# Performance work log

Measured on AMD Instinct MI355X. Metric: run time of the kernel, lower is better.

## Reference

```python
import jax, jax.numpy as jnp
import numpy as np

N = 50000
E = 800000
IN_C = 128
HID = 32
OUT_C = 16
NEG_SLOPE = 0.2


def setup_inputs() -> dict:
    key = jax.random.key(0)
    ks = jax.random.split(key, 16)
    x = jax.random.normal(ks[0], (N, IN_C), dtype=jnp.float32)
    edge_index = jax.random.randint(ks[1], (2, E), 0, N, dtype=jnp.int64)

    def glorot(k, shape):
        fan = shape[0] + shape[-1]
        return jax.random.uniform(k, shape, jnp.float32, -1.0, 1.0) * jnp.sqrt(6.0 / fan)

    # layer1: in=128 -> heads=4, ch=32, concat -> out 128
    W1 = glorot(ks[2], (IN_C, 4 * HID))
    a_src1 = glorot(ks[3], (4, HID))
    a_dst1 = glorot(ks[4], (4, HID))
    b1 = jnp.zeros((4 * HID,), jnp.float32)
    # layer2: in=128 -> heads=2, ch=32, concat -> out 64
    W2 = glorot(ks[5], (4 * HID, 2 * HID))
    a_src2 = glorot(ks[6], (2, HID))
    a_dst2 = glorot(ks[7], (2, HID))
    b2 = jnp.zeros((2 * HID,), jnp.float32)
    # layer3: in=64 -> heads=1, ch=16, mean -> out 16
    W3 = glorot(ks[8], (2 * HID, OUT_C))
    a_src3 = glorot(ks[9], (1, OUT_C))
    a_dst3 = glorot(ks[10], (1, OUT_C))
    b3 = jnp.zeros((OUT_C,), jnp.float32)
    return {"x": x, "edge_index": edge_index,
            "W1": W1, "a_src1": a_src1, "a_dst1": a_dst1, "b1": b1,
            "W2": W2, "a_src2": a_src2, "a_dst2": a_dst2, "b2": b2,
            "W3": W3, "a_src3": a_src3, "a_dst3": a_dst3, "b3": b3}


def gat_conv(x, src, dst, W, a_src, a_dst, bias, heads, ch, concat):
    n = x.shape[0]
    h = (x @ W).reshape(n, heads, ch)                      # [N,H,C]
    alpha_s = jnp.einsum('nhc,hc->nh', h, a_src)           # [N,H]
    alpha_d = jnp.einsum('nhc,hc->nh', h, a_dst)           # [N,H]
    logits = jax.nn.leaky_relu(alpha_s[src] + alpha_d[dst], NEG_SLOPE)  # [E,H]
    # segment softmax over edges sharing the same destination node
    m = jax.ops.segment_max(logits, dst, num_segments=n)
    m = jnp.where(jnp.isfinite(m), m, 0.0)
    e = jnp.exp(logits - m[dst])
    denom = jax.ops.segment_sum(e, dst, num_segments=n)
    alpha = e / (denom[dst] + 1e-16)                       # [E,H]
    msg = h[src] * alpha[:, :, None]                       # [E,H,C]
    out = jax.ops.segment_sum(msg, dst, num_segments=n)    # [N,H,C]
    out = out.reshape(n, heads * ch) if concat else out.mean(axis=1)
    return out + bias


def reference(x, edge_index, W1, a_src1, a_dst1, b1, W2, a_src2, a_dst2, b2, W3, a_src3, a_dst3, b3):
    n = x.shape[0]
    loops = jnp.arange(n, dtype=edge_index.dtype)
    src = jnp.concatenate([edge_index[0], loops])  # add self loops (PyG default)
    dst = jnp.concatenate([edge_index[1], loops])
    h = jax.nn.relu(gat_conv(x, src, dst, W1, a_src1, a_dst1, b1, 4, HID, True))
    h = jax.nn.relu(gat_conv(h, src, dst, W2, a_src2, a_dst2, b2, 2, HID, True))
    out = gat_conv(h, src, dst, W3, a_src3, a_dst3, b3, 1, OUT_C, False)
    return out
```

## Files before the change

### kernel.cpp

```cpp
#include <hip/hip_runtime.h>
#include <hip/hip_bf16.h>
#include <stdint.h>

#define NODES 50000
#define NEDGE 800000
#define TEDGE (NEDGE + NODES)

typedef unsigned short u16;
typedef unsigned int u32;
typedef unsigned long long u64;
typedef short s16x8 __attribute__((ext_vector_type(8)));
typedef float f32x4 __attribute__((ext_vector_type(4)));

__device__ __forceinline__ float bf2f(u16 v) {
  return __uint_as_float(((u32)v) << 16);
}
__device__ __forceinline__ u16 f2bf(float f) {
  u32 u = __float_as_uint(f);
  u32 r = (u + 0x7FFFu + ((u >> 16) & 1u)) >> 16;
  return (u16)r;
}
__device__ __forceinline__ float lrelu(float x) {
  return (x > 0.f) ? x : 0.2f * x;
}
__device__ __forceinline__ int clampn(int v) {
  return ((u32)v < NODES) ? v : 0;
}
__device__ __forceinline__ float load1(const void* p, size_t i, bool fb) {
  return fb ? bf2f(((const u16*)p)[i]) : ((const float*)p)[i];
}
__device__ __forceinline__ float bflo(u32 w) { return __uint_as_float(w << 16); }
__device__ __forceinline__ float bfhi(u32 w) { return __uint_as_float(w & 0xFFFF0000u); }
__device__ __forceinline__ u32 encf(float f) {
  u32 u = __float_as_uint(f);
  return (u & 0x80000000u) ? ~u : (u | 0x80000000u);
}
__device__ __forceinline__ float decf(u32 k) {
  u32 u = (k & 0x80000000u) ? (k & 0x7FFFFFFFu) : ~k;
  return __uint_as_float(u);
}
__device__ __forceinline__ void fma8(float* ac, uint4 v, float a) {
  ac[0] += a * bflo(v.x); ac[1] += a * bfhi(v.x);
  ac[2] += a * bflo(v.y); ac[3] += a * bfhi(v.y);
  ac[4] += a * bflo(v.z); ac[5] += a * bfhi(v.z);
  ac[6] += a * bflo(v.w); ac[7] += a * bfhi(v.w);
}

__global__ __launch_bounds__(256) void k_probe(const int* __restrict__ ei,
                                               const u16* __restrict__ xs16,
                                               int* __restrict__ flags,
                                               int* __restrict__ deg) {
  int t = threadIdx.x;
  int g = blockIdx.x * 256 + t;
  if (g < NODES) deg[g] = 0;
  if (blockIdx.x == 0 && t >= 2 && t < 32) flags[t] = 0;
  if (blockIdx.x == 0 && t < 64) {
    int odd = 0, even = 0, big = 0;
#pragma unroll
    for (int k = 0; k < 4; ++k) {
      int idx = t + 64 * k;
      odd |= (ei[2 * idx + 1] != 0);
      even |= (ei[2 * idx] != 0);
      u32 ex = (xs16[2 * (t * 4 + k)] >> 7) & 0xFF;
      big += (ex >= 0x90);
    }
    u64 bo = __ballot(odd);
    u64 be = __ballot(even);
#pragma unroll
    for (int off = 32; off >= 1; off >>= 1) big += __shfl_xor(big, off);
    if (t == 0) {
      flags[0] = (bo == 0ull && be != 0ull) ? 1 : 0;
      flags[1] = (big >= 8) ? 0 : 1;
    }
  }
}

__global__ __launch_bounds__(256) void k_tw(const void* __restrict__ W1,
                                            const void* __restrict__ W2,
                                            const void* __restrict__ W3,
                                            const int* __restrict__ flags,
                                            u16* __restrict__ wt1,
                                            u16* __restrict__ wt2,
                                            u16* __restrict__ wt3) {
  int id = blockIdx.x * 256 + threadIdx.x;
  bool fb = flags[1] != 0;
  if (id < 16384) {
    int n = id >> 7, k = id & 127;
    wt1[n * 128 + k] = f2bf(load1(W1, (size_t)k * 128 + n, fb));
  } else if (id < 24576) {
    int r = id - 16384;
    int n = r >> 7, k = r & 127;
    wt2[n * 128 + k] = f2bf(load1(W2, (size_t)k * 64 + n, fb));
  } else if (id < 25600) {
    int r = id - 24576;
    int n = r >> 6, k = r & 63;
    wt3[n * 64 + k] = f2bf(load1(W3, (size_t)k * 16 + n, fb));
  }
}


__global__ __launch_bounds__(256) void k_hist(const int* __restrict__ ei,
                                              const int* __restrict__ flags,
                                              int* deg, u16* __restrict__ rankarr) {
  int e = blockIdx.x * 256 + threadIdx.x;
  if (e >= TEDGE) return;
  int d;
  if (e < NEDGE) {
    d = flags[0] ? ei[2 * (NEDGE + e)] : ei[NEDGE + e];
  } else {
    d = e - NEDGE;
  }
  int r = atomicAdd(&deg[clampn(d)], 1);
  rankarr[e] = (u16)min(r, 65535);
}

__global__ __launch_bounds__(1024) void k_scan(const int* __restrict__ deg,
                                               int* __restrict__ rowptr, int n) {
  int t = threadIdx.x, lane = t & 63, w = t >> 6;
  __shared__ int swave[16], soff[17];
  int carry = 0;
  for (int base = 0; base < n; base += 4096) {
    int i0 = base + t * 4;
    int v[4];
#pragma unroll
    for (int j = 0; j < 4; j++) { int i = i0 + j; v[j] = (i < n) ? deg[i] : 0; }
    int local = v[0] + v[1] + v[2] + v[3];
    int x = local;
#pragma unroll
    for (int off = 1; off < 64; off <<= 1) {
      int y = __shfl_up(x, off);
      if (lane >= off) x += y;
    }
    if (lane == 63) swave[w] = x;
    __syncthreads();
    if (w == 0) {
      int wv = (lane < 16) ? swave[lane] : 0;
#pragma unroll
      for (int off = 1; off < 16; off <<= 1) {
        int y = __shfl_up(wv, off);
        if (lane >= off) wv += y;
      }
      if (lane < 16) soff[lane + 1] = wv;
      if (lane == 0) soff[0] = 0;
    }
    __syncthreads();
    int run = carry + soff[w] + (x - local);
#pragma unroll
    for (int j = 0; j < 4; j++) {
      int i = i0 + j;
      if (i < n) rowptr[i] = run;
      run += v[j];
    }
    carry += soff[16];
    __syncthreads();
  }
  if (t == 0) rowptr[n] = carry;
}

__global__ __launch_bounds__(256) void k_scatter(const int* __restrict__ ei,
                                                 const int* __restrict__ flags,
                                                 const int* __restrict__ rowptr,
                                                 const u16* __restrict__ rankarr,
                                                 u16* __restrict__ srcs) {
  int e = blockIdx.x * 256 + threadIdx.x;
  if (e >= TEDGE) return;
  int d, s;
  if (e < NEDGE) {
    if (flags[0]) { s = ei[2 * e]; d = ei[2 * (NEDGE + e)]; }
    else { s = ei[e]; d = ei[NEDGE + e]; }
  } else {
    s = e - NEDGE; d = s;
  }
  int pos = rowptr[clampn(d)] + (int)rankarr[e];
  srcs[pos] = (u16)clampn(s);
}


template <int K, int N, int H, bool XEXT>
__global__ __launch_bounds__(256) void k_gmfma(const void* __restrict__ xin,
                                               const u16* __restrict__ wtg,
                                               const void* __restrict__ a_src,
                                               const void* __restrict__ a_dst,
                                               u16* __restrict__ hout,
                                               float* __restrict__ asg,
                                               float* __restrict__ adg,
                                               u32* __restrict__ gm,
                                               const int* __restrict__ flags,
                                               int M) {
  constexpr int KP = K + 8;
  constexpr int NT = N / 16;
  constexpr int NTH = NT / H;
  constexpr int KG = K / 8;
  __shared__ u16 wlds[N * KP];
  __shared__ u16 xlds[64 * KP];
  __shared__ u32 lmax[2 * H];
  int t = threadIdx.x;
  int row0 = blockIdx.x * 64;
  bool fb = flags[1] != 0;
  if (t < 2 * H) lmax[t] = 0;

  for (int i = t; i < N * KG; i += 256) {
    int n = i / KG, kg = i % KG;
    *(uint4*)&wlds[n * KP + kg * 8] = *(const uint4*)(wtg + (size_t)n * K + kg * 8);
  }
  bool xbf = XEXT ? fb : true;
  for (int i = t; i < 64 * KG; i += 256) {
    int r = i / KG, kg = i % KG;
    int grow = row0 + r;
    if (grow >= M) grow = M - 1;
    if (xbf) {
      *(uint4*)&xlds[r * KP + kg * 8] =
          *(const uint4*)((const u16*)xin + (size_t)grow * K + kg * 8);
    } else {
      const float* gp = (const float*)xin + (size_t)grow * K + kg * 8;
      float4 f0 = *(const float4*)gp, f1 = *(const float4*)(gp + 4);
      *(ushort4*)&xlds[r * KP + kg * 8] =
          make_ushort4(f2bf(f0.x), f2bf(f0.y), f2bf(f0.z), f2bf(f0.w));
      *(ushort4*)&xlds[r * KP + kg * 8 + 4] =
          make_ushort4(f2bf(f1.x), f2bf(f1.y), f2bf(f1.z), f2bf(f1.w));
    }
  }
  __syncthreads();

  int lane = t & 63, w = t >> 6;
  int lrow = lane & 15, quad = lane >> 4;
  f32x4 acc[NT];
#pragma unroll
  for (int nt = 0; nt < NT; ++nt) acc[nt] = (f32x4){0.f, 0.f, 0.f, 0.f};

  const u16* xbase = xlds + (w * 16 + lrow) * KP + quad * 8;
  const u16* wbase = wlds + lrow * KP + quad * 8;
#pragma unroll
  for (int ks = 0; ks < K / 32; ++ks) {
    s16x8 a = *(const s16x8*)(xbase + ks * 32);
#pragma unroll
    for (int nt = 0; nt < NT; ++nt) {
      s16x8 b = *(const s16x8*)(wbase + (size_t)nt * 16 * KP + ks * 32);
      acc[nt] = __builtin_amdgcn_mfma_f32_16x16x32_bf16(a, b, acc[nt], 0, 0, 0);
    }
  }

  float avs[NT], avd[NT];
#pragma unroll
  for (int nt = 0; nt < NT; ++nt) {
    avs[nt] = load1(a_src, nt * 16 + lrow, fb);
    avd[nt] = load1(a_dst, nt * 16 + lrow, fb);
  }
  int baserow = row0 + w * 16 + quad * 4;
#pragma unroll
  for (int r = 0; r < 4; ++r) {
    int grow = baserow + r;
    float ps[H], pd[H];
#pragma unroll
    for (int h = 0; h < H; ++h) {
      ps[h] = 0.f; pd[h] = 0.f;
#pragma unroll
      for (int i = 0; i < NTH; ++i) {
        int nt = h * NTH + i;
        ps[h] += acc[nt][r] * avs[nt];
        pd[h] += acc[nt][r] * avd[nt];
      }
    }
#pragma unroll
    for (int m = 1; m < 16; m <<= 1) {
#pragma unroll
      for (int h = 0; h < H; ++h) {
        ps[h] += __shfl_xor(ps[h], m);
        pd[h] += __shfl_xor(pd[h], m);
      }
    }
    if (grow < M) {
#pragma unroll
      for (int nt = 0; nt < NT; ++nt)
        hout[(size_t)grow * N + nt * 16 + lrow] = f2bf(acc[nt][r]);
#pragma unroll
      for (int h = 0; h < H; ++h) {
        if (lrow == h) {
          asg[grow * H + h] = ps[h];
          adg[grow * H + h] = pd[h];
          atomicMax(&lmax[h], encf(ps[h]));
          atomicMax(&lmax[H + h], encf(pd[h]));
        }
      }
    }
  }
  __syncthreads();
  if (t < 2 * H) atomicMax(&gm[t], lmax[t]);
}


template <int H, int C, bool RELU, bool FINAL>
__global__ __launch_bounds__(256) void k_agg(const u16* __restrict__ hbuf,
                                             const float* __restrict__ asg,
                                             const float* __restrict__ adg,
                                             const int* __restrict__ rowptr,
                                             const u16* __restrict__ srcs,
                                             const void* __restrict__ bias,
                                             const int* __restrict__ flags,
                                             const u32* __restrict__ gm,
                                             void* __restrict__ outp, int n) {
  constexpr int HC = H * C;
  constexpr int L = HC / 8;
  constexpr int EPN = 32 / L;
  constexpr int UN = (4 * EPN <= 32) ? 4 : 2;
  __shared__ u16 lds_s[4][64];
  __shared__ float lds_e[4][64][H];
  int lane = threadIdx.x & 63;
  int w = threadIdx.x >> 6;
  int nh = lane >> 5;
  int hl = lane & 31;
  int node = blockIdx.x * 8 + w * 2 + nh;
  if (node >= n) node = n - 1;
  bool fb = flags[1] != 0;
  int start = rowptr[node], end = rowptr[node + 1];
  if (end < start || end - start > TEDGE) { start = 0; end = 0; }

  float adh[H], M[H];
#pragma unroll
  for (int h = 0; h < H; ++h) adh[h] = adg[node * H + h];
#pragma unroll
  for (int h = 0; h < H; ++h) M[h] = lrelu(decf(gm[h]) + decf(gm[H + h]));

  int sub = hl / L;
  int cl = hl & (L - 1);
  int ch0 = cl * 8;
  int myhead = ch0 / C;
  int base = nh * 32;

  float den[H];
#pragma unroll
  for (int h = 0; h < H; ++h) den[h] = 0.f;
  float acc[UN][8];
#pragma unroll
  for (int u = 0; u < UN; ++u)
#pragma unroll
    for (int i = 0; i < 8; ++i) acc[u][i] = 0.f;

  for (int chunk = start; chunk < end; chunk += 32) {
    int e = chunk + hl;
    int s = 0;
    float ee[H];
#pragma unroll
    for (int h = 0; h < H; ++h) ee[h] = 0.f;
    if (e < end) {
      s = srcs[e];
      float av[H];
      if (H == 4) { float4 t4 = *(const float4*)(asg + s * 4);
        av[0] = t4.x; av[1] = t4.y; av[H > 2 ? 2 : 0] = t4.z; av[H > 3 ? 3 : 0] = t4.w; }
      else if (H == 2) { float2 t2 = *(const float2*)(asg + s * 2); av[0] = t2.x; av[1] = t2.y; }
      else av[0] = asg[s];
#pragma unroll
      for (int h = 0; h < H; ++h) {
        float x = __expf(lrelu(av[h] + adh[h]) - M[h]);
        ee[h] = x;
        den[h] += x;
      }
    }
    __builtin_amdgcn_wave_barrier();
    lds_s[w][lane] = (u16)s;
#pragma unroll
    for (int h = 0; h < H; ++h) lds_e[w][lane][h] = ee[h];
    __builtin_amdgcn_wave_barrier();

    int cn = min(32, end - chunk);
    for (int j = 0; j < cn; j += UN * EPN) {
      int sx[UN];
      float ax[UN];
#pragma unroll
      for (int u = 0; u < UN; ++u) {
        int ei_ = base + j + u * EPN + sub;
        sx[u] = lds_s[w][ei_];
        ax[u] = lds_e[w][ei_][myhead];
      }
#pragma unroll
      for (int u = 0; u < UN; ++u) {
        uint4 v = *(const uint4*)(hbuf + (size_t)sx[u] * HC + ch0);
        fma8(acc[u], v, ax[u]);
      }
    }
  }

#pragma unroll
  for (int m = 16; m >= 1; m >>= 1) {
#pragma unroll
    for (int h = 0; h < H; ++h) den[h] += __shfl_xor(den[h], m);
  }
  float tt[8];
#pragma unroll
  for (int i = 0; i < 8; ++i) {
    tt[i] = acc[0][i];
#pragma unroll
    for (int u = 1; u < UN; ++u) tt[i] += acc[u][i];
  }
#pragma unroll
  for (int m = L; m < 32; m <<= 1) {
#pragma unroll
    for (int i = 0; i < 8; ++i) tt[i] += __shfl_xor(tt[i], m);
  }

  if (sub == 0) {
    float inv = 1.f / (den[myhead] + 1e-16f);
    float o[8];
#pragma unroll
    for (int i = 0; i < 8; ++i) {
      o[i] = tt[i] * inv + load1(bias, ch0 + i, fb);
      if (RELU) o[i] = fmaxf(o[i], 0.f);
    }
    bool obf = FINAL ? fb : true;
    if (obf) {
      uint4 pk;
      pk.x = (u32)f2bf(o[0]) | ((u32)f2bf(o[1]) << 16);
      pk.y = (u32)f2bf(o[2]) | ((u32)f2bf(o[3]) << 16);
      pk.z = (u32)f2bf(o[4]) | ((u32)f2bf(o[5]) << 16);
      pk.w = (u32)f2bf(o[6]) | ((u32)f2bf(o[7]) << 16);
      *(uint4*)((u16*)outp + (size_t)node * HC + ch0) = pk;
    } else {
      float* op = (float*)outp + (size_t)node * HC + ch0;
      *(float4*)op = make_float4(o[0], o[1], o[2], o[3]);
      *(float4*)(op + 4) = make_float4(o[4], o[5], o[6], o[7]);
    }
  }
}


extern "C" void kernel_launch(void* const* d_in, const int* in_sizes, int n_in,
                              void* d_out, int out_size, void* d_ws, size_t ws_size,
                              hipStream_t stream) {
  const void* x   = d_in[0];
  const int* ei   = (const int*)d_in[1];
  const void* W1  = d_in[2];
  const void* as1 = d_in[3];
  const void* ad1 = d_in[4];
  const void* b1  = d_in[5];
  const void* W2  = d_in[6];
  const void* as2 = d_in[7];
  const void* ad2 = d_in[8];
  const void* b2  = d_in[9];
  const void* W3  = d_in[10];
  const void* as3 = d_in[11];
  const void* ad3 = d_in[12];
  const void* b3  = d_in[13];

  char* w = (char*)d_ws;
  auto alloc = [&](size_t bytes) {
    char* p = w;
    w += (bytes + 255) & ~(size_t)255;
    return p;
  };
  int* flags    = (int*)alloc(256);
  int* deg      = (int*)alloc((size_t)NODES * 4);
  int* rowptr   = (int*)alloc((size_t)(NODES + 1) * 4);
  u16* rankarr  = (u16*)alloc((size_t)TEDGE * 2);
  u16* srcs     = (u16*)alloc((size_t)TEDGE * 2);
  float* asg    = (float*)alloc((size_t)NODES * 4 * 4);
  float* adg    = (float*)alloc((size_t)NODES * 4 * 4);
  u16* wt1      = (u16*)alloc((size_t)128 * 128 * 2);
  u16* wt2      = (u16*)alloc((size_t)64 * 128 * 2);
  u16* wt3      = (u16*)alloc((size_t)16 * 64 * 2);
  u16* hbuf     = (u16*)alloc((size_t)NODES * 128 * 2);
  u16* obuf     = (u16*)alloc((size_t)NODES * 128 * 2);

  u32* gm1 = (u32*)(flags + 8);
  u32* gm2 = (u32*)(flags + 16);
  u32* gm3 = (u32*)(flags + 24);

  k_probe<<<(NODES + 255) / 256, 256, 0, stream>>>(ei, (const u16*)x, flags, deg);
  k_tw<<<100, 256, 0, stream>>>(W1, W2, W3, flags, wt1, wt2, wt3);
  k_hist<<<(TEDGE + 255) / 256, 256, 0, stream>>>(ei, flags, deg, rankarr);
  k_scan<<<1, 1024, 0, stream>>>(deg, rowptr, NODES);
  k_scatter<<<(TEDGE + 255) / 256, 256, 0, stream>>>(ei, flags, rowptr, rankarr, srcs);

  int gblocks = (NODES + 63) / 64;
  int ablocks = (NODES + 7) / 8;
  k_gmfma<128, 128, 4, true><<<gblocks, 256, 0, stream>>>(x, wt1, as1, ad1, hbuf, asg, adg, gm1, flags, NODES);
  k_agg<4, 32, true, false><<<ablocks, 256, 0, stream>>>(hbuf, asg, adg, rowptr, srcs, b1, flags, gm1, obuf, NODES);
  k_gmfma<128, 64, 2, false><<<gblocks, 256, 0, stream>>>(obuf, wt2, as2, ad2, hbuf, asg, adg, gm2, flags, NODES);
  k_agg<2, 32, true, false><<<ablocks, 256, 0, stream>>>(hbuf, asg, adg, rowptr, srcs, b2, flags, gm2, obuf, NODES);
  k_gmfma<64, 16, 1, false><<<gblocks, 256, 0, stream>>>(obuf, wt3, as3, ad3, hbuf, asg, adg, gm3, flags, NODES);
  k_agg<1, 16, false, true><<<ablocks, 256, 0, stream>>>(hbuf, asg, adg, rowptr, srcs, b3, flags, gm3, d_out, NODES);
}
```

Measured before the change: 310.4 us.

## Switch intermediates to fp16 MFMA and cache compact edge indices for scatter

Moves the weight, projected-feature and intermediate activation buffers from bf16 to fp16, so the GEMMs use the f16 MFMA variant and aggregation decodes fp16 halves, which gives more mantissa precision. The histogram kernel now writes clamped 16-bit source and destination arrays, so the scatter pass reads 4 bytes per edge instead of re-reading the 64-bit edge_index. This adds two extra writes per edge in k_hist and a float conversion cost per element in the aggregation loop. fp16 also risks overflow if activations grow large.

```diff
diff --git a/kernel.cpp b/kernel.cpp
--- a/kernel.cpp
+++ b/kernel.cpp
@@ -9,7 +9,8 @@
 typedef unsigned short u16;
 typedef unsigned int u32;
 typedef unsigned long long u64;
-typedef short s16x8 __attribute__((ext_vector_type(8)));
+typedef _Float16 f16;
+typedef _Float16 f16x8 __attribute__((ext_vector_type(8)));
 typedef float f32x4 __attribute__((ext_vector_type(4)));
 
 __device__ __forceinline__ float bf2f(u16 v) {
@@ -20,6 +21,18 @@
   u32 r = (u + 0x7FFFu + ((u >> 16) & 1u)) >> 16;
   return (u16)r;
 }
+__device__ __forceinline__ u16 f2h(float f) {
+  return __builtin_bit_cast(u16, (f16)f);
+}
+__device__ __forceinline__ float h2f(u16 b) {
+  return (float)__builtin_bit_cast(f16, b);
+}
+__device__ __forceinline__ float lo16f(u32 w) {
+  return (float)__builtin_bit_cast(f16, (u16)(w & 0xFFFFu));
+}
+__device__ __forceinline__ float hi16f(u32 w) {
+  return (float)__builtin_bit_cast(f16, (u16)(w >> 16));
+}
 __device__ __forceinline__ float lrelu(float x) {
   return (x > 0.f) ? x : 0.2f * x;
 }
@@ -29,8 +42,6 @@
 __device__ __forceinline__ float load1(const void* p, size_t i, bool fb) {
   return fb ? bf2f(((const u16*)p)[i]) : ((const float*)p)[i];
 }
-__device__ __forceinline__ float bflo(u32 w) { return __uint_as_float(w << 16); }
-__device__ __forceinline__ float bfhi(u32 w) { return __uint_as_float(w & 0xFFFF0000u); }
 __device__ __forceinline__ u32 encf(float f) {
   u32 u = __float_as_uint(f);
   return (u & 0x80000000u) ? ~u : (u | 0x80000000u);
@@ -39,11 +50,11 @@
   u32 u = (k & 0x80000000u) ? (k & 0x7FFFFFFFu) : ~k;
   return __uint_as_float(u);
 }
-__device__ __forceinline__ void fma8(float* ac, uint4 v, float a) {
-  ac[0] += a * bflo(v.x); ac[1] += a * bfhi(v.x);
-  ac[2] += a * bflo(v.y); ac[3] += a * bfhi(v.y);
-  ac[4] += a * bflo(v.z); ac[5] += a * bfhi(v.z);
-  ac[6] += a * bflo(v.w); ac[7] += a * bfhi(v.w);
+__device__ __forceinline__ void fma8h(float* ac, uint4 v, float a) {
+  ac[0] += a * lo16f(v.x); ac[1] += a * hi16f(v.x);
+  ac[2] += a * lo16f(v.y); ac[3] += a * hi16f(v.y);
+  ac[4] += a * lo16f(v.z); ac[5] += a * hi16f(v.z);
+  ac[6] += a * lo16f(v.w); ac[7] += a * hi16f(v.w);
 }
 
 __global__ __launch_bounds__(256) void k_probe(const int* __restrict__ ei,
@@ -86,31 +97,37 @@
   bool fb = flags[1] != 0;
   if (id < 16384) {
     int n = id >> 7, k = id & 127;
-    wt1[n * 128 + k] = f2bf(load1(W1, (size_t)k * 128 + n, fb));
+    wt1[n * 128 + k] = f2h(load1(W1, (size_t)k * 128 + n, fb));
   } else if (id < 24576) {
     int r = id - 16384;
     int n = r >> 7, k = r & 127;
-    wt2[n * 128 + k] = f2bf(load1(W2, (size_t)k * 64 + n, fb));
+    wt2[n * 128 + k] = f2h(load1(W2, (size_t)k * 64 + n, fb));
   } else if (id < 25600) {
     int r = id - 24576;
     int n = r >> 6, k = r & 63;
-    wt3[n * 64 + k] = f2bf(load1(W3, (size_t)k * 16 + n, fb));
+    wt3[n * 64 + k] = f2h(load1(W3, (size_t)k * 16 + n, fb));
   }
 }
 
 
 __global__ __launch_bounds__(256) void k_hist(const int* __restrict__ ei,
                                               const int* __restrict__ flags,
-                                              int* deg, u16* __restrict__ rankarr) {
+                                              int* deg, u16* __restrict__ rankarr,
+                                              u16* __restrict__ src16,
+                                              u16* __restrict__ dst16) {
   int e = blockIdx.x * 256 + threadIdx.x;
   if (e >= TEDGE) return;
-  int d;
+  int d, s;
   if (e < NEDGE) {
-    d = flags[0] ? ei[2 * (NEDGE + e)] : ei[NEDGE + e];
+    if (flags[0]) { s = ei[2 * e]; d = ei[2 * (NEDGE + e)]; }
+    else { s = ei[e]; d = ei[NEDGE + e]; }
   } else {
-    d = e - NEDGE;
-  }
-  int r = atomicAdd(&deg[clampn(d)], 1);
+    s = e - NEDGE; d = s;
+  }
+  s = clampn(s); d = clampn(d);
+  src16[e] = (u16)s;
+  dst16[e] = (u16)d;
+  int r = atomicAdd(&deg[d], 1);
   rankarr[e] = (u16)min(r, 65535);
 }
 
@@ -157,22 +174,16 @@
   if (t == 0) rowptr[n] = carry;
 }
 
-__global__ __launch_bounds__(256) void k_scatter(const int* __restrict__ ei,
-                                                 const int* __restrict__ flags,
+__global__ __launch_bounds__(256) void k_scatter(const u16* __restrict__ src16,
+                                                 const u16* __restrict__ dst16,
                                                  const int* __restrict__ rowptr,
                                                  const u16* __restrict__ rankarr,
                                                  u16* __restrict__ srcs) {
   int e = blockIdx.x * 256 + threadIdx.x;
   if (e >= TEDGE) return;
-  int d, s;
-  if (e < NEDGE) {
-    if (flags[0]) { s = ei[2 * e]; d = ei[2 * (NEDGE + e)]; }
-    else { s = ei[e]; d = ei[NEDGE + e]; }
-  } else {
-    s = e - NEDGE; d = s;
-  }
-  int pos = rowptr[clampn(d)] + (int)rankarr[e];
-  srcs[pos] = (u16)clampn(s);
+  int d = dst16[e];
+  int pos = rowptr[d] + (int)rankarr[e];
+  srcs[pos] = src16[e];
 }
 
 
@@ -203,21 +214,29 @@
     int n = i / KG, kg = i % KG;
     *(uint4*)&wlds[n * KP + kg * 8] = *(const uint4*)(wtg + (size_t)n * K + kg * 8);
   }
-  bool xbf = XEXT ? fb : true;
   for (int i = t; i < 64 * KG; i += 256) {
     int r = i / KG, kg = i % KG;
     int grow = row0 + r;
     if (grow >= M) grow = M - 1;
-    if (xbf) {
+    if (XEXT) {
+      if (fb) {
+        const u16* gp = (const u16*)xin + (size_t)grow * K + kg * 8;
+        ushort4 v0 = *(const ushort4*)gp, v1 = *(const ushort4*)(gp + 4);
+        *(ushort4*)&xlds[r * KP + kg * 8] = make_ushort4(
+            f2h(bf2f(v0.x)), f2h(bf2f(v0.y)), f2h(bf2f(v0.z)), f2h(bf2f(v0.w)));
+        *(ushort4*)&xlds[r * KP + kg * 8 + 4] = make_ushort4(
+            f2h(bf2f(v1.x)), f2h(bf2f(v1.y)), f2h(bf2f(v1.z)), f2h(bf2f(v1.w)));
+      } else {
+        const float* gp = (const float*)xin + (size_t)grow * K + kg * 8;
+        float4 f0 = *(const float4*)gp, f1 = *(const float4*)(gp + 4);
+        *(ushort4*)&xlds[r * KP + kg * 8] =
+            make_ushort4(f2h(f0.x), f2h(f0.y), f2h(f0.z), f2h(f0.w));
+        *(ushort4*)&xlds[r * KP + kg * 8 + 4] =
+            make_ushort4(f2h(f1.x), f2h(f1.y), f2h(f1.z), f2h(f1.w));
+      }
+    } else {
       *(uint4*)&xlds[r * KP + kg * 8] =
           *(const uint4*)((const u16*)xin + (size_t)grow * K + kg * 8);
-    } else {
-      const float* gp = (const float*)xin + (size_t)grow * K + kg * 8;
-      float4 f0 = *(const float4*)gp, f1 = *(const float4*)(gp + 4);
-      *(ushort4*)&xlds[r * KP + kg * 8] =
-          make_ushort4(f2bf(f0.x), f2bf(f0.y), f2bf(f0.z), f2bf(f0.w));
-      *(ushort4*)&xlds[r * KP + kg * 8 + 4] =
-          make_ushort4(f2bf(f1.x), f2bf(f1.y), f2bf(f1.z), f2bf(f1.w));
     }
   }
   __syncthreads();
@@ -232,11 +251,11 @@
   const u16* wbase = wlds + lrow * KP + quad * 8;
 #pragma unroll
   for (int ks = 0; ks < K / 32; ++ks) {
-    s16x8 a = *(const s16x8*)(xbase + ks * 32);
+    f16x8 a = *(const f16x8*)(xbase + ks * 32);
 #pragma unroll
     for (int nt = 0; nt < NT; ++nt) {
-      s16x8 b = *(const s16x8*)(wbase + (size_t)nt * 16 * KP + ks * 32);
-      acc[nt] = __builtin_amdgcn_mfma_f32_16x16x32_bf16(a, b, acc[nt], 0, 0, 0);
+      f16x8 b = *(const f16x8*)(wbase + (size_t)nt * 16 * KP + ks * 32);
+      acc[nt] = __builtin_amdgcn_mfma_f32_16x16x32_f16(a, b, acc[nt], 0, 0, 0);
     }
   }
 
@@ -272,7 +291,7 @@
     if (grow < M) {
 #pragma unroll
       for (int nt = 0; nt < NT; ++nt)
-        hout[(size_t)grow * N + nt * 16 + lrow] = f2bf(acc[nt][r]);
+        hout[(size_t)grow * N + nt * 16 + lrow] = f2h(acc[nt][r]);
 #pragma unroll
       for (int h = 0; h < H; ++h) {
         if (lrow == h) {
@@ -375,7 +394,7 @@
 #pragma unroll
       for (int u = 0; u < UN; ++u) {
         uint4 v = *(const uint4*)(hbuf + (size_t)sx[u] * HC + ch0);
-        fma8(acc[u], v, ax[u]);
+        fma8h(acc[u], v, ax[u]);
       }
     }
   }
@@ -406,18 +425,26 @@
       o[i] = tt[i] * inv + load1(bias, ch0 + i, fb);
       if (RELU) o[i] = fmaxf(o[i], 0.f);
     }
-    bool obf = FINAL ? fb : true;
-    if (obf) {
+    if (FINAL) {
+      if (fb) {
+        uint4 pk;
+        pk.x = (u32)f2bf(o[0]) | ((u32)f2bf(o[1]) << 16);
+        pk.y = (u32)f2bf(o[2]) | ((u32)f2bf(o[3]) << 16);
+        pk.z = (u32)f2bf(o[4]) | ((u32)f2bf(o[5]) << 16);
+        pk.w = (u32)f2bf(o[6]) | ((u32)f2bf(o[7]) << 16);
+        *(uint4*)((u16*)outp + (size_t)node * HC + ch0) = pk;
+      } else {
+        float* op = (float*)outp + (size_t)node * HC + ch0;
+        *(float4*)op = make_float4(o[0], o[1], o[2], o[3]);
+        *(float4*)(op + 4) = make_float4(o[4], o[5], o[6], o[7]);
+      }
+    } else {
       uint4 pk;
-      pk.x = (u32)f2bf(o[0]) | ((u32)f2bf(o[1]) << 16);
-      pk.y = (u32)f2bf(o[2]) | ((u32)f2bf(o[3]) << 16);
-      pk.z = (u32)f2bf(o[4]) | ((u32)f2bf(o[5]) << 16);
-      pk.w = (u32)f2bf(o[6]) | ((u32)f2bf(o[7]) << 16);
+      pk.x = (u32)f2h(o[0]) | ((u32)f2h(o[1]) << 16);
+      pk.y = (u32)f2h(o[2]) | ((u32)f2h(o[3]) << 16);
+      pk.z = (u32)f2h(o[4]) | ((u32)f2h(o[5]) << 16);
+      pk.w = (u32)f2h(o[6]) | ((u32)f2h(o[7]) << 16);
       *(uint4*)((u16*)outp + (size_t)node * HC + ch0) = pk;
-    } else {
-      float* op = (float*)outp + (size_t)node * HC + ch0;
-      *(float4*)op = make_float4(o[0], o[1], o[2], o[3]);
-      *(float4*)(op + 4) = make_float4(o[4], o[5], o[6], o[7]);
     }
   }
 }
@@ -451,6 +478,8 @@
   int* deg      = (int*)alloc((size_t)NODES * 4);
   int* rowptr   = (int*)alloc((size_t)(NODES + 1) * 4);
   u16* rankarr  = (u16*)alloc((size_t)TEDGE * 2);
+  u16* src16    = (u16*)alloc((size_t)TEDGE * 2);
+  u16* dst16    = (u16*)alloc((size_t)TEDGE * 2);
   u16* srcs     = (u16*)alloc((size_t)TEDGE * 2);
   float* asg    = (float*)alloc((size_t)NODES * 4 * 4);
   float* adg    = (float*)alloc((size_t)NODES * 4 * 4);
@@ -466,9 +495,9 @@
 
   k_probe<<<(NODES + 255) / 256, 256, 0, stream>>>(ei, (const u16*)x, flags, deg);
   k_tw<<<100, 256, 0, stream>>>(W1, W2, W3, flags, wt1, wt2, wt3);
-  k_hist<<<(TEDGE + 255) / 256, 256, 0, stream>>>(ei, flags, deg, rankarr);
+  k_hist<<<(TEDGE + 255) / 256, 256, 0, stream>>>(ei, flags, deg, rankarr, src16, dst16);
   k_scan<<<1, 1024, 0, stream>>>(deg, rowptr, NODES);
-  k_scatter<<<(TEDGE + 255) / 256, 256, 0, stream>>>(ei, flags, rowptr, rankarr, srcs);
+  k_scatter<<<(TEDGE + 255) / 256, 256, 0, stream>>>(src16, dst16, rowptr, rankarr, srcs);
 
   int gblocks = (NODES + 63) / 64;
   int ablocks = (NODES + 7) / 8;
```

New measurement: 316.2 us. About the same (+1.8%).
